# Kernel optimization log

Hardware: AMD Instinct MI355X
Metric: run time of the kernel (lower is better)

## Reference

```python
import jax, jax.numpy as jnp
import numpy as np

K_NEIGHBORS = 8
OVERLAP_THRESHOLD = 0.1
LAMBDA_RECON, LAMBDA_PERCEP, LAMBDA_CONT, LAMBDA_BND = 1.0, 0.5, 0.5, 1.0


def _cdist(x, y):
    x2 = jnp.sum(x * x, axis=-1)
    y2 = jnp.sum(y * y, axis=-1)
    sq = x2[..., :, None] + y2[..., None, :] - 2.0 * jnp.einsum('...nd,...md->...nm', x, y)
    return jnp.sqrt(jnp.maximum(sq, 0.0))


def _continuity_loss(points, k=K_NEIGHBORS):
    # points: [B, N, 3]
    d = jax.lax.stop_gradient(_cdist(points, points))  # indices only, no grad through dists
    _, idx = jax.lax.top_k(-d, k + 1)                  # ascending distance, [B, N, k+1]
    idx = idx[:, :, 1:]                                # drop self, [B, N, k]
    # gather neighbors: [B, N, k, 3]
    neighbors = jnp.take_along_axis(points[:, None, :, :], idx[..., None], axis=2)
    mean = neighbors.mean(axis=2, keepdims=True)
    return jnp.mean(jnp.sum((neighbors - mean) ** 2, axis=-1))


def _boundary_loss(c1, c2, thr=OVERLAP_THRESHOLD):
    min_d = _cdist(c1, c2).min(axis=1)                 # [M1]
    mask = min_d < thr
    cnt = jnp.sum(mask)
    s = jnp.sum(jnp.where(mask, min_d, 0.0))
    return jnp.where(cnt > 0, s / jnp.maximum(cnt, 1).astype(min_d.dtype), 0.0)


def setup_inputs() -> dict:
    key = jax.random.key(0)
    ks = jax.random.split(key, 6)
    B, N = 4, 8192
    return {
        'predicted': jax.random.normal(ks[0], (B, N, 3), jnp.float32),
        'target': jax.random.normal(ks[1], (B, N, 3), jnp.float32),
        'predicted_features': jax.random.normal(ks[2], (B, 1024), jnp.float32),
        'target_features': jax.random.normal(ks[3], (B, 1024), jnp.float32),
        'chunk1': jax.random.uniform(ks[4], (4096, 3), jnp.float32),
        'chunk2': jax.random.uniform(ks[5], (4096, 3), jnp.float32),
    }


def reference(predicted, target, predicted_features, target_features, chunk1, chunk2):
    recon = jnp.mean((predicted - target) ** 2)
    percep = jnp.mean((predicted_features - target_features) ** 2)
    cont = _continuity_loss(predicted)
    bnd = _boundary_loss(chunk1, chunk2)  # single chunk pair -> mean of one boundary loss
    total = LAMBDA_RECON * recon + LAMBDA_PERCEP * percep + LAMBDA_CONT * cont + LAMBDA_BND * bnd
    return recon, percep, cont, bnd, total
```

## Files before the change

### kernel.cpp

```cpp
#include <hip/hip_runtime.h>
#include <math.h>

#define NBATCH 4
#define NPTS   8192
#define KNN    8
#define NCH    4096
#define SLICES 16
#define SLEN   512
#define NWIN   8
#define WLEN   64
#define CTR_OFF 64
#define PB_OFF  256
#define C2_OFF  (PB_OFF + NBATCH * (NPTS / 2) * 12)
#define NAUX   114

typedef float    v2f __attribute__((ext_vector_type(2)));
typedef _Float16 v2h __attribute__((ext_vector_type(2)));

__device__ __forceinline__ unsigned umin32(unsigned a, unsigned b) { return a < b ? a : b; }
__device__ __forceinline__ unsigned h2u(v2h v) { unsigned u; __builtin_memcpy(&u, &v, 4); return u; }
__device__ __forceinline__ v2h u2h(unsigned u) { v2h v; __builtin_memcpy(&v, &u, 4); return v; }

#define INSERT8(bd, key)                                          \
    asm("v_med3_u32 %7, %8, %6, %7\n\t"                           \
        "v_med3_u32 %6, %8, %5, %6\n\t"                           \
        "v_med3_u32 %5, %8, %4, %5\n\t"                           \
        "v_med3_u32 %4, %8, %3, %4\n\t"                           \
        "v_med3_u32 %3, %8, %2, %3\n\t"                           \
        "v_med3_u32 %2, %8, %1, %2\n\t"                           \
        "v_med3_u32 %1, %8, %0, %1\n\t"                           \
        "v_min_u32  %0, %0, %8"                                   \
        : "+v"(bd[0]), "+v"(bd[1]), "+v"(bd[2]), "+v"(bd[3]),     \
          "+v"(bd[4]), "+v"(bd[5]), "+v"(bd[6]), "+v"(bd[7])      \
        : "v"(key))

__global__ __launch_bounds__(256) void prep_kernel(const float* __restrict__ pts,
                                                   const float* __restrict__ c2,
                                                   unsigned* __restrict__ pb16,
                                                   float* __restrict__ c2p,
                                                   double* __restrict__ acc,
                                                   unsigned* __restrict__ ctr) {
    const int gi = blockIdx.x * 256 + threadIdx.x;
    if (gi < 8) acc[gi] = 0.0;
    if (gi == 8) *ctr = 0u;
    if (gi < NBATCH * NPTS / 2) {
        const float* s = pts + (size_t)gi * 6;
        const v2h xp = {(_Float16)s[0], (_Float16)s[3]};
        const v2h yp = {(_Float16)s[1], (_Float16)s[4]};
        const v2h zp = {(_Float16)s[2], (_Float16)s[5]};
        pb16[gi * 3 + 0] = h2u(xp);
        pb16[gi * 3 + 1] = h2u(yp);
        pb16[gi * 3 + 2] = h2u(zp);
    } else {
        const int pi = gi - NBATCH * NPTS / 2;
        const float* s = c2 + (size_t)pi * 6;
        const float x0 = s[0], y0 = s[1], z0 = s[2];
        const float x1 = s[3], y1 = s[4], z1 = s[5];
        float4* o = reinterpret_cast<float4*>(c2p + (size_t)pi * 8);
        o[0] = make_float4(x0, x1, y0, y1);
        o[1] = make_float4(z0, z1, x0 * x0 + y0 * y0 + z0 * z0,
                                   x1 * x1 + y1 * y1 + z1 * z1);
    }
}

__global__ __launch_bounds__(1024, 8) void cont_kernel(const unsigned* __restrict__ pb16,
                                                       const float* __restrict__ pred,
                                                       double* __restrict__ acc) {
    __shared__ unsigned mrg[SLICES][KNN][64];
    const int t    = threadIdx.x;
    const int lane = t & 63;
    const int w    = __builtin_amdgcn_readfirstlane(t >> 6);
    const int nqw  = NPTS / 64;
    const int b    = blockIdx.x / nqw;
    const int q0   = (blockIdx.x % nqw) * 64;
    const unsigned* __restrict__ B = pb16 + (size_t)b * (NPTS / 2) * 3;

    const int qi = q0 + lane;
    const unsigned* qp = B + (size_t)(qi >> 1) * 3;
    const int e = qi & 1;
    const v2h xqv = u2h(qp[0]), yqv = u2h(qp[1]), zqv = u2h(qp[2]);
    const _Float16 qxh = xqv[e], qyh = yqv[e], qzh = zqv[e];
    const v2h qx2 = {qxh, qxh}, qy2 = {qyh, qyh}, qz2 = {qzh, qzh};

    const unsigned* __restrict__ Sp = B + (size_t)w * (SLEN / 2) * 3;
    const unsigned jb = (unsigned)(w * SLEN);
    unsigned keyout[NWIN];

#pragma unroll
    for (int wi = 0; wi < NWIN; ++wi) {
        const unsigned* __restrict__ Wp = Sp + wi * ((WLEN / 2) * 3);
        unsigned wmA = 0xFFFFFFFFu, wmB = 0xFFFFFFFFu;
#pragma unroll
        for (int j = 0; j < WLEN / 2; ++j) {
            const v2h xh = u2h(Wp[j * 3 + 0]);
            const v2h yh = u2h(Wp[j * 3 + 1]);
            const v2h zh = u2h(Wp[j * 3 + 2]);
            const v2h dx = xh - qx2;
            const v2h dy = yh - qy2;
            const v2h dz = zh - qz2;
            v2h d2 = dx * dx;
            d2 = __builtin_elementwise_fma(dy, dy, d2);
            d2 = __builtin_elementwise_fma(dz, dz, d2);
            const unsigned bits = h2u(d2);
            const unsigned k0 = (bits << 16) | (unsigned)(2 * j);
            const unsigned k1 = (bits & 0xFFFF0000u) | (unsigned)(2 * j + 1);
            wmA = umin32(wmA, k0);
            wmB = umin32(wmB, k1);
        }
        const unsigned wm = umin32(wmA, wmB);
        keyout[wi] = (wm & 0xFFFF0000u) | (jb + (unsigned)(wi * WLEN)) | (wm & 63u);
    }

#pragma unroll
    for (int wi = 0; wi < NWIN; ++wi) mrg[w][wi][lane] = keyout[wi];
    __syncthreads();

    if (w < 4) {
        const unsigned selfidx = (unsigned)qi;
        unsigned best[KNN];
#pragma unroll
        for (int s = 0; s < KNN; ++s) best[s] = 0xFFFFFFFFu;
        for (int sl = 4 * w; sl < 4 * w + 4; ++sl) {
#pragma unroll
            for (int u = 0; u < KNN; ++u) {
                unsigned key = mrg[sl][u][lane];
                key = ((key & 0x1FFFu) == selfidx) ? 0xFFFFFFFFu : key;
                INSERT8(best, key);
            }
        }
#pragma unroll
        for (int s = 0; s < KNN; ++s) mrg[4 * w][s][lane] = best[s];
    }
    __syncthreads();

    if (w == 0) {
        unsigned best[KNN];
#pragma unroll
        for (int s = 0; s < KNN; ++s) best[s] = 0xFFFFFFFFu;
        for (int g = 0; g < 4; ++g) {
#pragma unroll
            for (int u = 0; u < KNN; ++u) {
                const unsigned key = mrg[4 * g][u][lane];
                INSERT8(best, key);
            }
        }
        const float* __restrict__ P = pred + (size_t)b * NPTS * 3;
        float sx = 0.f, sy = 0.f, sz = 0.f, sw = 0.f;
#pragma unroll
        for (int s = 0; s < KNN; ++s) {
            const unsigned n = best[s] & 0x1FFFu;
            const float* np = P + (size_t)n * 3;
            const float x = np[0], y = np[1], z = np[2];
            sx += x; sy += y; sz += z;
            sw += x * x + y * y + z * z;
        }
        float ssum = sw - (sx * sx + sy * sy + sz * sz) * (1.f / KNN);
#pragma unroll
        for (int o = 32; o > 0; o >>= 1) ssum += __shfl_down(ssum, o, 64);
        if (lane == 0) atomicAdd(&acc[2], (double)ssum);
    }
}

__global__ __launch_bounds__(512) void aux_kernel(const float* __restrict__ a,
                                                  const float* __restrict__ bt,
                                                  const float* __restrict__ a2,
                                                  const float* __restrict__ b2,
                                                  const float* __restrict__ c1,
                                                  const float* __restrict__ c2p,
                                                  double* __restrict__ acc,
                                                  unsigned* __restrict__ ctr,
                                                  float* __restrict__ out) {
    __shared__ float smem[8 * 64];
    const int t = threadIdx.x;
    const int blk = blockIdx.x;
    if (blk < 50) {
        float s;
        int which;
        if (blk < 48) {
            which = 0;
            const int i = blk * 512 + t;
            const float4 va = reinterpret_cast<const float4*>(a)[i];
            const float4 vb = reinterpret_cast<const float4*>(bt)[i];
            const float dx = va.x - vb.x, dy = va.y - vb.y;
            const float dz = va.z - vb.z, dw = va.w - vb.w;
            s = dx * dx + dy * dy + dz * dz + dw * dw;
        } else {
            which = 1;
            const int i = (blk - 48) * 512 + t;
            const float4 va = reinterpret_cast<const float4*>(a2)[i];
            const float4 vb = reinterpret_cast<const float4*>(b2)[i];
            const float dx = va.x - vb.x, dy = va.y - vb.y;
            const float dz = va.z - vb.z, dw = va.w - vb.w;
            s = dx * dx + dy * dy + dz * dz + dw * dw;
        }
#pragma unroll
        for (int o = 32; o > 0; o >>= 1) s += __shfl_down(s, o, 64);
        if ((t & 63) == 0) smem[t >> 6] = s;
        __syncthreads();
        if (t == 0) {
            float bs = 0.f;
#pragma unroll
            for (int i = 0; i < 8; ++i) bs += smem[i];
            atomicAdd(&acc[which], (double)bs);
        }
    } else {
        const int lane = t & 63;
        const int w8 = __builtin_amdgcn_readfirstlane(t >> 6);
        const int qi = (blk - 50) * 64 + lane;
        const float qx = c1[qi * 3 + 0];
        const float qy = c1[qi * 3 + 1];
        const float qz = c1[qi * 3 + 2];
        const float qn = qx * qx + qy * qy + qz * qz;
        const v2f m2x2 = {-2.f * qx, -2.f * qx};
        const v2f m2y2 = {-2.f * qy, -2.f * qy};
        const v2f m2z2 = {-2.f * qz, -2.f * qz};
        float m = 3.0e38f;
        const float* __restrict__ Sp = c2p + (size_t)w8 * 256 * 8;
#pragma unroll 16
        for (int j = 0; j < 256; ++j) {
            const float4 ab = *reinterpret_cast<const float4*>(Sp + j * 8);
            const float4 cd = *reinterpret_cast<const float4*>(Sp + j * 8 + 4);
            const v2f xp = {ab.x, ab.y}, yp = {ab.z, ab.w};
            const v2f zp = {cd.x, cd.y};
            v2f s2 = {cd.z, cd.w};
            s2 = __builtin_elementwise_fma(zp, m2z2, s2);
            s2 = __builtin_elementwise_fma(yp, m2y2, s2);
            s2 = __builtin_elementwise_fma(xp, m2x2, s2);
            m = fminf(m, fminf(s2.x, s2.y));
        }
        smem[w8 * 64 + lane] = m;
        __syncthreads();
        if (w8 == 0) {
            float mm = smem[lane];
#pragma unroll
            for (int s = 1; s < 8; ++s) mm = fminf(mm, smem[s * 64 + lane]);
            const float d = sqrtf(fmaxf(mm + qn, 0.f));
            const bool in = d < 0.1f;
            float sc = in ? d : 0.f;
            float sn = in ? 1.f : 0.f;
#pragma unroll
            for (int o = 32; o > 0; o >>= 1) {
                sc += __shfl_down(sc, o, 64);
                sn += __shfl_down(sn, o, 64);
            }
            if (lane == 0) {
                atomicAdd(&acc[3], (double)sc);
                atomicAdd(&acc[4], (double)sn);
            }
        }
    }
    __syncthreads();
    if (t == 0) {
        __threadfence();
        const unsigned old = atomicAdd(ctr, 1u);
        if (old == NAUX - 1) {
            __threadfence();
            const double a0 = atomicAdd(&acc[0], 0.0);
            const double a1 = atomicAdd(&acc[1], 0.0);
            const double a2d = atomicAdd(&acc[2], 0.0);
            const double a3 = atomicAdd(&acc[3], 0.0);
            const double a4 = atomicAdd(&acc[4], 0.0);
            const double recon  = a0 / (double)(NBATCH * NPTS * 3);
            const double percep = a1 / 4096.0;
            const double cont   = a2d / (double)(NBATCH * NPTS * KNN);
            const double bnd    = (a4 > 0.0) ? a3 / ((a4 > 1.0) ? a4 : 1.0) : 0.0;
            const double total  = recon + 0.5 * percep + 0.5 * cont + bnd;
            out[0] = (float)recon;
            out[1] = (float)percep;
            out[2] = (float)cont;
            out[3] = (float)bnd;
            out[4] = (float)total;
        }
    }
}

extern "C" void kernel_launch(void* const* d_in, const int* in_sizes, int n_in,
                              void* d_out, int out_size, void* d_ws, size_t ws_size,
                              hipStream_t stream) {
    const float* pred = (const float*)d_in[0];
    const float* targ = (const float*)d_in[1];
    const float* pf   = (const float*)d_in[2];
    const float* tf   = (const float*)d_in[3];
    const float* c1   = (const float*)d_in[4];
    const float* c2   = (const float*)d_in[5];
    float* out  = (float*)d_out;
    double* acc = (double*)d_ws;
    unsigned* ctr = (unsigned*)((char*)d_ws + CTR_OFF);
    unsigned* pb16 = (unsigned*)((char*)d_ws + PB_OFF);
    float* c2p  = (float*)((char*)d_ws + C2_OFF);

    hipLaunchKernelGGL(prep_kernel, dim3((NBATCH * NPTS / 2 + NCH / 2) / 256), dim3(256),
                       0, stream, pred, c2, pb16, c2p, acc, ctr);
    hipLaunchKernelGGL(cont_kernel, dim3(NBATCH * (NPTS / 64)), dim3(1024), 0, stream,
                       pb16, pred, acc);
    hipLaunchKernelGGL(aux_kernel, dim3(NAUX), dim3(512), 0, stream,
                       pred, targ, pf, tf, c1, c2p, acc, ctr, out);
}
```

Before: 71.24 us.

## Switch kNN scan to fp32 norm-expansion and fuse boundary into main kernel

Replaces the fp16 packed point layout with a fp32 layout carrying x,y,z pairs plus squared norms, and computes kNN distances through the norm expansion with FMAs, two windows interleaved per iteration for more ILP. The recon and perceptual reductions move into the prep kernel, and the boundary-loss blocks are merged into the kNN kernel, cutting launches from three kernels to a memset plus two. This doubles the bytes read in the scan and adds fp32 work, but gains precision in neighbour selection and removes one kernel launch and its tail.

New measurement: 91.72 us. 1.29x slower.

```diff
diff --git a/kernel.cpp b/kernel.cpp
--- a/kernel.cpp
+++ b/kernel.cpp
@@ -9,17 +9,16 @@
 #define SLEN   512
 #define NWIN   8
 #define WLEN   64
-#define CTR_OFF 64
+#define CTR_OFF 56
 #define PB_OFF  256
-#define C2_OFF  (PB_OFF + NBATCH * (NPTS / 2) * 12)
-#define NAUX   114
-
-typedef float    v2f __attribute__((ext_vector_type(2)));
-typedef _Float16 v2h __attribute__((ext_vector_type(2)));
+#define C2_OFF  (PB_OFF + NBATCH * (NPTS / 2) * 32)
+#define BND_BLOCKS  32
+#define SCAN_BLOCKS (NBATCH * (NPTS / 64))
+#define TOT_BLOCKS  (BND_BLOCKS + SCAN_BLOCKS)
+
+typedef float v2f __attribute__((ext_vector_type(2)));
 
 __device__ __forceinline__ unsigned umin32(unsigned a, unsigned b) { return a < b ? a : b; }
-__device__ __forceinline__ unsigned h2u(v2h v) { unsigned u; __builtin_memcpy(&u, &v, 4); return u; }
-__device__ __forceinline__ v2h u2h(unsigned u) { v2h v; __builtin_memcpy(&v, &u, 4); return v; }
 
 #define INSERT8(bd, key)                                          \
     asm("v_med3_u32 %7, %8, %6, %7\n\t"                           \
@@ -34,179 +33,96 @@
           "+v"(bd[4]), "+v"(bd[5]), "+v"(bd[6]), "+v"(bd[7])      \
         : "v"(key))
 
-__global__ __launch_bounds__(256) void prep_kernel(const float* __restrict__ pts,
+#define PAIR_EVAL(PTR, J, wm0, wm1)                                          \
+    do {                                                                     \
+        const float4 ab = *reinterpret_cast<const float4*>((PTR) + (J) * 8); \
+        const float4 cd = *reinterpret_cast<const float4*>((PTR) + (J) * 8 + 4); \
+        const v2f xp = {ab.x, ab.y}, yp = {ab.z, ab.w};                      \
+        const v2f zp = {cd.x, cd.y};                                         \
+        v2f s2 = {cd.z, cd.w};                                               \
+        s2 += qnp2;                                                          \
+        s2 = __builtin_elementwise_fma(zp, m2z2, s2);                        \
+        s2 = __builtin_elementwise_fma(yp, m2y2, s2);                        \
+        s2 = __builtin_elementwise_fma(xp, m2x2, s2);                        \
+        wm0 = umin32(wm0, (__float_as_uint(s2.x) & 0xFFFFFFC0u) | (unsigned)(2 * (J))); \
+        wm1 = umin32(wm1, (__float_as_uint(s2.y) & 0xFFFFFFC0u) | (unsigned)(2 * (J) + 1)); \
+    } while (0)
+
+__global__ __launch_bounds__(512) void prep_kernel(const float* __restrict__ pts,
                                                    const float* __restrict__ c2,
-                                                   unsigned* __restrict__ pb16,
+                                                   const float* __restrict__ a,
+                                                   const float* __restrict__ bt,
+                                                   const float* __restrict__ a2,
+                                                   const float* __restrict__ b2,
+                                                   float* __restrict__ pb,
                                                    float* __restrict__ c2p,
-                                                   double* __restrict__ acc,
-                                                   unsigned* __restrict__ ctr) {
-    const int gi = blockIdx.x * 256 + threadIdx.x;
-    if (gi < 8) acc[gi] = 0.0;
-    if (gi == 8) *ctr = 0u;
-    if (gi < NBATCH * NPTS / 2) {
-        const float* s = pts + (size_t)gi * 6;
-        const v2h xp = {(_Float16)s[0], (_Float16)s[3]};
-        const v2h yp = {(_Float16)s[1], (_Float16)s[4]};
-        const v2h zp = {(_Float16)s[2], (_Float16)s[5]};
-        pb16[gi * 3 + 0] = h2u(xp);
-        pb16[gi * 3 + 1] = h2u(yp);
-        pb16[gi * 3 + 2] = h2u(zp);
-    } else {
-        const int pi = gi - NBATCH * NPTS / 2;
-        const float* s = c2 + (size_t)pi * 6;
+                                                   double* __restrict__ acc) {
+    __shared__ float red[8];
+    const int t = threadIdx.x;
+    const int blk = blockIdx.x;
+    if (blk < 36) {
+        const float* src;
+        float* dst;
+        int pi;
+        if (blk < 32) { src = pts; dst = pb; pi = blk * 512 + t; }
+        else { src = c2; dst = c2p; pi = (blk - 32) * 512 + t; }
+        const float* s = src + (size_t)pi * 6;
         const float x0 = s[0], y0 = s[1], z0 = s[2];
         const float x1 = s[3], y1 = s[4], z1 = s[5];
-        float4* o = reinterpret_cast<float4*>(c2p + (size_t)pi * 8);
+        float4* o = reinterpret_cast<float4*>(dst + (size_t)pi * 8);
         o[0] = make_float4(x0, x1, y0, y1);
         o[1] = make_float4(z0, z1, x0 * x0 + y0 * y0 + z0 * z0,
                                    x1 * x1 + y1 * y1 + z1 * z1);
+        return;
+    }
+    float s;
+    int which;
+    if (blk < 84) {
+        which = 0;
+        const int i = (blk - 36) * 512 + t;
+        const float4 va = reinterpret_cast<const float4*>(a)[i];
+        const float4 vb = reinterpret_cast<const float4*>(bt)[i];
+        const float dx = va.x - vb.x, dy = va.y - vb.y;
+        const float dz = va.z - vb.z, dw = va.w - vb.w;
+        s = dx * dx + dy * dy + dz * dz + dw * dw;
+    } else {
+        which = 1;
+        const int i = (blk - 84) * 512 + t;
+        const float4 va = reinterpret_cast<const float4*>(a2)[i];
+        const float4 vb = reinterpret_cast<const float4*>(b2)[i];
+        const float dx = va.x - vb.x, dy = va.y - vb.y;
+        const float dz = va.z - vb.z, dw = va.w - vb.w;
+        s = dx * dx + dy * dy + dz * dz + dw * dw;
+    }
+#pragma unroll
+    for (int o = 32; o > 0; o >>= 1) s += __shfl_down(s, o, 64);
+    if ((t & 63) == 0) red[t >> 6] = s;
+    __syncthreads();
+    if (t == 0) {
+        float bs = 0.f;
+#pragma unroll
+        for (int i = 0; i < 8; ++i) bs += red[i];
+        atomicAdd(&acc[which], (double)bs);
     }
 }
 
-__global__ __launch_bounds__(1024, 8) void cont_kernel(const unsigned* __restrict__ pb16,
+__global__ __launch_bounds__(1024, 8) void main_kernel(const float* __restrict__ pb,
                                                        const float* __restrict__ pred,
-                                                       double* __restrict__ acc) {
+                                                       const float* __restrict__ c1,
+                                                       const float* __restrict__ c2p,
+                                                       double* __restrict__ acc,
+                                                       unsigned* __restrict__ ctr,
+                                                       float* __restrict__ out) {
     __shared__ unsigned mrg[SLICES][KNN][64];
     const int t    = threadIdx.x;
     const int lane = t & 63;
     const int w    = __builtin_amdgcn_readfirstlane(t >> 6);
-    const int nqw  = NPTS / 64;
-    const int b    = blockIdx.x / nqw;
-    const int q0   = (blockIdx.x % nqw) * 64;
-    const unsigned* __restrict__ B = pb16 + (size_t)b * (NPTS / 2) * 3;
-
-    const int qi = q0 + lane;
-    const unsigned* qp = B + (size_t)(qi >> 1) * 3;
-    const int e = qi & 1;
-    const v2h xqv = u2h(qp[0]), yqv = u2h(qp[1]), zqv = u2h(qp[2]);
-    const _Float16 qxh = xqv[e], qyh = yqv[e], qzh = zqv[e];
-    const v2h qx2 = {qxh, qxh}, qy2 = {qyh, qyh}, qz2 = {qzh, qzh};
-
-    const unsigned* __restrict__ Sp = B + (size_t)w * (SLEN / 2) * 3;
-    const unsigned jb = (unsigned)(w * SLEN);
-    unsigned keyout[NWIN];
-
-#pragma unroll
-    for (int wi = 0; wi < NWIN; ++wi) {
-        const unsigned* __restrict__ Wp = Sp + wi * ((WLEN / 2) * 3);
-        unsigned wmA = 0xFFFFFFFFu, wmB = 0xFFFFFFFFu;
-#pragma unroll
-        for (int j = 0; j < WLEN / 2; ++j) {
-            const v2h xh = u2h(Wp[j * 3 + 0]);
-            const v2h yh = u2h(Wp[j * 3 + 1]);
-            const v2h zh = u2h(Wp[j * 3 + 2]);
-            const v2h dx = xh - qx2;
-            const v2h dy = yh - qy2;
-            const v2h dz = zh - qz2;
-            v2h d2 = dx * dx;
-            d2 = __builtin_elementwise_fma(dy, dy, d2);
-            d2 = __builtin_elementwise_fma(dz, dz, d2);
-            const unsigned bits = h2u(d2);
-            const unsigned k0 = (bits << 16) | (unsigned)(2 * j);
-            const unsigned k1 = (bits & 0xFFFF0000u) | (unsigned)(2 * j + 1);
-            wmA = umin32(wmA, k0);
-            wmB = umin32(wmB, k1);
-        }
-        const unsigned wm = umin32(wmA, wmB);
-        keyout[wi] = (wm & 0xFFFF0000u) | (jb + (unsigned)(wi * WLEN)) | (wm & 63u);
-    }
-
-#pragma unroll
-    for (int wi = 0; wi < NWIN; ++wi) mrg[w][wi][lane] = keyout[wi];
-    __syncthreads();
-
-    if (w < 4) {
-        const unsigned selfidx = (unsigned)qi;
-        unsigned best[KNN];
-#pragma unroll
-        for (int s = 0; s < KNN; ++s) best[s] = 0xFFFFFFFFu;
-        for (int sl = 4 * w; sl < 4 * w + 4; ++sl) {
-#pragma unroll
-            for (int u = 0; u < KNN; ++u) {
-                unsigned key = mrg[sl][u][lane];
-                key = ((key & 0x1FFFu) == selfidx) ? 0xFFFFFFFFu : key;
-                INSERT8(best, key);
-            }
-        }
-#pragma unroll
-        for (int s = 0; s < KNN; ++s) mrg[4 * w][s][lane] = best[s];
-    }
-    __syncthreads();
-
-    if (w == 0) {
-        unsigned best[KNN];
-#pragma unroll
-        for (int s = 0; s < KNN; ++s) best[s] = 0xFFFFFFFFu;
-        for (int g = 0; g < 4; ++g) {
-#pragma unroll
-            for (int u = 0; u < KNN; ++u) {
-                const unsigned key = mrg[4 * g][u][lane];
-                INSERT8(best, key);
-            }
-        }
-        const float* __restrict__ P = pred + (size_t)b * NPTS * 3;
-        float sx = 0.f, sy = 0.f, sz = 0.f, sw = 0.f;
-#pragma unroll
-        for (int s = 0; s < KNN; ++s) {
-            const unsigned n = best[s] & 0x1FFFu;
-            const float* np = P + (size_t)n * 3;
-            const float x = np[0], y = np[1], z = np[2];
-            sx += x; sy += y; sz += z;
-            sw += x * x + y * y + z * z;
-        }
-        float ssum = sw - (sx * sx + sy * sy + sz * sz) * (1.f / KNN);
-#pragma unroll
-        for (int o = 32; o > 0; o >>= 1) ssum += __shfl_down(ssum, o, 64);
-        if (lane == 0) atomicAdd(&acc[2], (double)ssum);
-    }
-}
-
-__global__ __launch_bounds__(512) void aux_kernel(const float* __restrict__ a,
-                                                  const float* __restrict__ bt,
-                                                  const float* __restrict__ a2,
-                                                  const float* __restrict__ b2,
-                                                  const float* __restrict__ c1,
-                                                  const float* __restrict__ c2p,
-                                                  double* __restrict__ acc,
-                                                  unsigned* __restrict__ ctr,
-                                                  float* __restrict__ out) {
-    __shared__ float smem[8 * 64];
-    const int t = threadIdx.x;
-    const int blk = blockIdx.x;
-    if (blk < 50) {
-        float s;
-        int which;
-        if (blk < 48) {
-            which = 0;
-            const int i = blk * 512 + t;
-            const float4 va = reinterpret_cast<const float4*>(a)[i];
-            const float4 vb = reinterpret_cast<const float4*>(bt)[i];
-            const float dx = va.x - vb.x, dy = va.y - vb.y;
-            const float dz = va.z - vb.z, dw = va.w - vb.w;
-            s = dx * dx + dy * dy + dz * dz + dw * dw;
-        } else {
-            which = 1;
-            const int i = (blk - 48) * 512 + t;
-            const float4 va = reinterpret_cast<const float4*>(a2)[i];
-            const float4 vb = reinterpret_cast<const float4*>(b2)[i];
-            const float dx = va.x - vb.x, dy = va.y - vb.y;
-            const float dz = va.z - vb.z, dw = va.w - vb.w;
-            s = dx * dx + dy * dy + dz * dz + dw * dw;
-        }
-#pragma unroll
-        for (int o = 32; o > 0; o >>= 1) s += __shfl_down(s, o, 64);
-        if ((t & 63) == 0) smem[t >> 6] = s;
-        __syncthreads();
-        if (t == 0) {
-            float bs = 0.f;
-#pragma unroll
-            for (int i = 0; i < 8; ++i) bs += smem[i];
-            atomicAdd(&acc[which], (double)bs);
-        }
-    } else {
-        const int lane = t & 63;
-        const int w8 = __builtin_amdgcn_readfirstlane(t >> 6);
-        const int qi = (blk - 50) * 64 + lane;
+
+    if (blockIdx.x < BND_BLOCKS) {
+        float* mn = (float*)mrg;
+        const int g  = w >> 3;
+        const int wg = w & 7;
+        const int qi = blockIdx.x * 128 + g * 64 + lane;
         const float qx = c1[qi * 3 + 0];
         const float qy = c1[qi * 3 + 1];
         const float qz = c1[qi * 3 + 2];
@@ -215,7 +131,7 @@
         const v2f m2y2 = {-2.f * qy, -2.f * qy};
         const v2f m2z2 = {-2.f * qz, -2.f * qz};
         float m = 3.0e38f;
-        const float* __restrict__ Sp = c2p + (size_t)w8 * 256 * 8;
+        const float* __restrict__ Sp = c2p + (size_t)wg * 256 * 8;
 #pragma unroll 16
         for (int j = 0; j < 256; ++j) {
             const float4 ab = *reinterpret_cast<const float4*>(Sp + j * 8);
@@ -228,12 +144,12 @@
             s2 = __builtin_elementwise_fma(xp, m2x2, s2);
             m = fminf(m, fminf(s2.x, s2.y));
         }
-        smem[w8 * 64 + lane] = m;
+        mn[(g * 8 + wg) * 64 + lane] = m;
         __syncthreads();
-        if (w8 == 0) {
-            float mm = smem[lane];
-#pragma unroll
-            for (int s = 1; s < 8; ++s) mm = fminf(mm, smem[s * 64 + lane]);
+        if (wg == 0) {
+            float mm = mn[g * 512 + lane];
+#pragma unroll
+            for (int s = 1; s < 8; ++s) mm = fminf(mm, mn[g * 512 + s * 64 + lane]);
             const float d = sqrtf(fmaxf(mm + qn, 0.f));
             const bool in = d < 0.1f;
             float sc = in ? d : 0.f;
@@ -248,12 +164,102 @@
                 atomicAdd(&acc[4], (double)sn);
             }
         }
-    }
+    } else {
+        const int blk2 = blockIdx.x - BND_BLOCKS;
+        const int nqw  = NPTS / 64;
+        const int b    = blk2 / nqw;
+        const int q0   = (blk2 % nqw) * 64;
+        const float* __restrict__ B = pb + (size_t)b * (NPTS / 2) * 8;
+
+        const int qi = q0 + lane;
+        const float* qp = B + (size_t)(qi >> 1) * 8;
+        const int e = qi & 1;
+        const float qx = qp[0 + e], qy = qp[2 + e], qz = qp[4 + e], qw = qp[6 + e];
+        const v2f qnp2 = {qw + 1e-6f, qw + 1e-6f};
+        const v2f m2x2 = {-2.f * qx, -2.f * qx};
+        const v2f m2y2 = {-2.f * qy, -2.f * qy};
+        const v2f m2z2 = {-2.f * qz, -2.f * qz};
+
+        const float* __restrict__ Sp = B + (size_t)w * SLEN * 4;
+        int voff = w * (SLEN * 4);
+        asm("" : "+v"(voff));
+        const float* __restrict__ Bv = B + voff;
+
+        const unsigned jb = (unsigned)(w * SLEN);
+        unsigned keyout[NWIN];
+
+#pragma unroll
+        for (int wp = 0; wp < 4; ++wp) {
+            const float* __restrict__ Ws = Sp + wp * (WLEN * 4);
+            const float* __restrict__ Wv = Bv + (wp + 4) * (WLEN * 4);
+            unsigned mS0 = 0xFFFFFFFFu, mS1 = 0xFFFFFFFFu;
+            unsigned mV0 = 0xFFFFFFFFu, mV1 = 0xFFFFFFFFu;
+#pragma unroll
+            for (int j = 0; j < WLEN / 2; ++j) {
+                PAIR_EVAL(Ws, j, mS0, mS1);
+                PAIR_EVAL(Wv, j, mV0, mV1);
+            }
+            const unsigned wmS = umin32(mS0, mS1);
+            const unsigned wmV = umin32(mV0, mV1);
+            keyout[wp]     = (wmS & 0xFFFFE000u) | (jb + (unsigned)(wp * WLEN)) | (wmS & 63u);
+            keyout[wp + 4] = (wmV & 0xFFFFE000u) | (jb + (unsigned)((wp + 4) * WLEN)) | (wmV & 63u);
+        }
+
+#pragma unroll
+        for (int wi = 0; wi < NWIN; ++wi) mrg[w][wi][lane] = keyout[wi];
+        __syncthreads();
+
+        if (w < 4) {
+            const unsigned selfidx = (unsigned)qi;
+            unsigned best[KNN];
+#pragma unroll
+            for (int s = 0; s < KNN; ++s) best[s] = 0xFFFFFFFFu;
+            for (int sl = 4 * w; sl < 4 * w + 4; ++sl) {
+#pragma unroll
+                for (int u = 0; u < KNN; ++u) {
+                    unsigned key = mrg[sl][u][lane];
+                    key = ((key & 0x1FFFu) == selfidx) ? 0xFFFFFFFFu : key;
+                    INSERT8(best, key);
+                }
+            }
+#pragma unroll
+            for (int s = 0; s < KNN; ++s) mrg[4 * w][s][lane] = best[s];
+        }
+        __syncthreads();
+
+        if (w == 0) {
+            unsigned best[KNN];
+#pragma unroll
+            for (int s = 0; s < KNN; ++s) best[s] = 0xFFFFFFFFu;
+            for (int g = 0; g < 4; ++g) {
+#pragma unroll
+                for (int u = 0; u < KNN; ++u) {
+                    const unsigned key = mrg[4 * g][u][lane];
+                    INSERT8(best, key);
+                }
+            }
+            const float* __restrict__ P = pred + (size_t)b * NPTS * 3;
+            float sx = 0.f, sy = 0.f, sz = 0.f, sw = 0.f;
+#pragma unroll
+            for (int s = 0; s < KNN; ++s) {
+                const unsigned n = best[s] & 0x1FFFu;
+                const float* np = P + (size_t)n * 3;
+                const float x = np[0], y = np[1], z = np[2];
+                sx += x; sy += y; sz += z;
+                sw += x * x + y * y + z * z;
+            }
+            float ssum = sw - (sx * sx + sy * sy + sz * sz) * (1.f / KNN);
+#pragma unroll
+            for (int o = 32; o > 0; o >>= 1) ssum += __shfl_down(ssum, o, 64);
+            if (lane == 0) atomicAdd(&acc[2], (double)ssum);
+        }
+    }
+
     __syncthreads();
     if (t == 0) {
         __threadfence();
         const unsigned old = atomicAdd(ctr, 1u);
-        if (old == NAUX - 1) {
+        if (old == TOT_BLOCKS - 1) {
             __threadfence();
             const double a0 = atomicAdd(&acc[0], 0.0);
             const double a1 = atomicAdd(&acc[1], 0.0);
@@ -286,13 +292,12 @@
     float* out  = (float*)d_out;
     double* acc = (double*)d_ws;
     unsigned* ctr = (unsigned*)((char*)d_ws + CTR_OFF);
-    unsigned* pb16 = (unsigned*)((char*)d_ws + PB_OFF);
+    float* pb   = (float*)((char*)d_ws + PB_OFF);
     float* c2p  = (float*)((char*)d_ws + C2_OFF);
 
-    hipLaunchKernelGGL(prep_kernel, dim3((NBATCH * NPTS / 2 + NCH / 2) / 256), dim3(256),
-                       0, stream, pred, c2, pb16, c2p, acc, ctr);
-    hipLaunchKernelGGL(cont_kernel, dim3(NBATCH * (NPTS / 64)), dim3(1024), 0, stream,
-                       pb16, pred, acc);
-    hipLaunchKernelGGL(aux_kernel, dim3(NAUX), dim3(512), 0, stream,
-                       pred, targ, pf, tf, c1, c2p, acc, ctr, out);
+    hipMemsetAsync(d_ws, 0, 64, stream);
+    hipLaunchKernelGGL(prep_kernel, dim3(86), dim3(512), 0, stream,
+                       pred, c2, pred, targ, pf, tf, pb, c2p, acc);
+    hipLaunchKernelGGL(main_kernel, dim3(TOT_BLOCKS), dim3(1024), 0, stream,
+                       pb, pred, c1, c2p, acc, ctr, out);
 }
```
